# Optimization experiments

Hardware: AMD Instinct MI355X
Metric: run time of the kernel (lower is better)

## Reference

```python
import jax, jax.numpy as jnp
import numpy as np

B, T, D_IN = 512, 128, 256
H1, H2 = 1024, 1024
LABEL_DIM = 3


def _lstm_layer(x, W, U, b):
    """Run one keras-LSTMCell layer over x: [T, B, D_in] -> [T, B, H].

    Keras gate order is (i, f, g, o); c' = f*c + i*tanh(g); h = o*tanh(c').
    """
    H = U.shape[0]
    batch = x.shape[1]

    def step(carry, xt):
        h, c = carry
        z = xt @ W + h @ U + b  # [B, 4H]
        i, f, g, o = jnp.split(z, 4, axis=-1)
        i = jax.nn.sigmoid(i)
        f = jax.nn.sigmoid(f)
        g = jnp.tanh(g)
        o = jax.nn.sigmoid(o)
        c_new = f * c + i * g
        h_new = o * jnp.tanh(c_new)
        return (h_new, c_new), h_new

    init = (jnp.zeros((batch, H), x.dtype), jnp.zeros((batch, H), x.dtype))
    _, hs = jax.lax.scan(step, init, x)
    return hs  # [T, B, H]


def setup_inputs() -> dict:
    key = jax.random.key(0)
    ks = jax.random.split(key, 10)
    chars = jax.random.normal(ks[0], (B, T, D_IN), dtype=jnp.float32)
    # sequence lengths in [1, T] so sequence_length - 1 is a valid index
    sequence_length = jax.random.randint(ks[1], (B,), 1, T + 1)
    s = 0.05
    W1 = jax.random.normal(ks[2], (D_IN, 4 * H1), dtype=jnp.float32) * s
    U1 = jax.random.normal(ks[3], (H1, 4 * H1), dtype=jnp.float32) * s
    b1 = jnp.zeros((4 * H1,), dtype=jnp.float32)
    W2 = jax.random.normal(ks[4], (H1, 4 * H2), dtype=jnp.float32) * s
    U2 = jax.random.normal(ks[5], (H2, 4 * H2), dtype=jnp.float32) * s
    b2 = jnp.zeros((4 * H2,), dtype=jnp.float32)
    Wd = jax.random.normal(ks[6], (H2, LABEL_DIM), dtype=jnp.float32) * s
    bd = jnp.zeros((LABEL_DIM,), dtype=jnp.float32)
    return {"chars": chars, "sequence_length": sequence_length,
            "W1": W1, "U1": U1, "b1": b1,
            "W2": W2, "U2": U2, "b2": b2,
            "Wd": Wd, "bd": bd}


def reference(chars, sequence_length, W1, U1, b1, W2, U2, b2, Wd, bd):
    # chars: [B, T, 256] -> time-major [T, B, 256]
    x = jnp.transpose(chars, (1, 0, 2))
    x = _lstm_layer(x, W1, U1, b1)          # [T, B, H1]
    x = _lstm_layer(x, W2, U2, b2)          # [T, B, H2]
    # gather the hidden state at the last valid timestep of each sequence
    batch = chars.shape[0]
    hidden = x[sequence_length - 1, jnp.arange(batch)]  # [B, H2]
    return jax.nn.relu(hidden @ Wd + bd)    # [B, label_dim]
```

## Files before the change

### kernel.cpp

```cpp
#include <hip/hip_runtime.h>
#include <hip/hip_bf16.h>


typedef __hip_bfloat16 bf16;
typedef __attribute__((ext_vector_type(8))) short bfrag8;
typedef __attribute__((ext_vector_type(4))) float accf4;

#define BATCH 512
#define TSTEPS 128
#define DIN 256
#define H 1024
#define NG 4096

__device__ __forceinline__ float sigm(float x) { return 1.0f / (1.0f + __expf(-x)); }
__device__ __forceinline__ float tanh_f(float x) {
    float a = fabsf(x);
    float e = __expf(-2.0f * a);
    float t = (1.0f - e) / (1.0f + e);
    return x < 0.0f ? -t : t;
}
__device__ __forceinline__ unsigned short bfr16(float x) {
    bf16 h = __float2bfloat16(x);
    return *(unsigned short*)&h;
}
__device__ __forceinline__ void gll16(const void* g, void* l) {
    __builtin_amdgcn_global_load_lds(
        (const __attribute__((address_space(1))) unsigned int*)g,
        (__attribute__((address_space(3))) unsigned int*)l, 16, 0, 0);
}

__global__ void k_repack(const float* __restrict__ W, const float* __restrict__ U,
                         bf16* __restrict__ Bp, int KIN)
{
    __shared__ float tile[128][65];
    int kt = blockIdx.x, nt = blockIdx.y;
    int lane = threadIdx.x;
    int n = nt * 64 + lane;
    int orig = ((n >> 4) & 3) * 1024 + (n >> 7) * 32 + ((n >> 6) & 1) * 16 + (n & 15);
    for (int j = 0; j < 128; ++j) {
        int k = kt * 128 + j;
        tile[j][lane] = (k < KIN) ? W[(size_t)k * NG + orig]
                                  : U[(size_t)(k - KIN) * NG + orig];
    }
    __syncthreads();
    for (int u = 0; u < 16; ++u) {
        int cid = u * 64 + lane;
        int nloc = cid >> 4;
        int pos = cid & 15;
        int nn = nt * 64 + nloc;
        int kc = pos ^ (nn & 7);
        alignas(16) unsigned short pk[8];
        #pragma unroll
        for (int jj = 0; jj < 8; ++jj) pk[jj] = bfr16(tile[kc * 8 + jj][nloc]);
        *(int4*)(Bp + ((size_t)kt * NG + nn) * 128 + pos * 8) = *(int4*)pk;
    }
}

struct StepJob {
    const float* Xf;
    const bf16* A0;
    const bf16* A1;
    const bf16* Bp;
    const float* bias;
    float* C;
    bf16* Hout;
    float* hidden;
    const int* seqlen;
    int xstride;
    int ksplit;
    int KT;
    int t;
};

__global__ __launch_bounds__(256, 2) void k_step(StepJob j0, StepJob j1)
{
    __shared__ __align__(16) bf16 Alds[64 * 128];
    __shared__ __align__(16) bf16 Blds[128 * 128];

    const StepJob jb = (blockIdx.x >> 8) ? j1 : j0;
    int bi = blockIdx.x & 255;
    int tid = threadIdx.x;
    int wv = tid >> 6, lane = tid & 63;
    int ntile = bi & 31;
    int b0 = (bi >> 5) * 64;
    int n0 = ntile * 128;
    int mw = (wv & 1) * 32;
    int nw = (wv >> 1) * 64;
    int c = lane & 15, q = lane >> 4;

    const accf4 zero4 = {0.f, 0.f, 0.f, 0.f};
    accf4 acc[2][4];
    #pragma unroll
    for (int i = 0; i < 2; ++i)
        #pragma unroll
        for (int j = 0; j < 4; ++j) acc[i][j] = zero4;

    for (int kt = 0; kt < jb.KT; ++kt) {
        int k0 = kt << 7;
        if (jb.Xf && k0 < jb.ksplit) {
            #pragma unroll
            for (int uu = 0; uu < 4; ++uu) {
                int u = uu * 256 + tid;
                int r = u >> 4;
                int pos = u & 15;
                int kc = pos ^ (r & 7);
                const float* src = jb.Xf + (size_t)(b0 + r) * jb.xstride + k0 + kc * 8;
                float4 va = *(const float4*)src;
                float4 vb = *(const float4*)(src + 4);
                alignas(16) unsigned short pk[8];
                pk[0] = bfr16(va.x); pk[1] = bfr16(va.y);
                pk[2] = bfr16(va.z); pk[3] = bfr16(va.w);
                pk[4] = bfr16(vb.x); pk[5] = bfr16(vb.y);
                pk[6] = bfr16(vb.z); pk[7] = bfr16(vb.w);
                *(int4*)((char*)Alds + u * 16) = *(int4*)pk;
            }
        } else {
            const bf16* Asrc; int kk0;
            if (k0 < jb.ksplit) { Asrc = jb.A0; kk0 = k0; }
            else                { Asrc = jb.A1; kk0 = k0 - jb.ksplit; }
            #pragma unroll
            for (int cc = 0; cc < 4; ++cc) {
                int ob = wv * 4096 + cc * 1024;
                int o = ob + lane * 16;
                int r = o >> 8;
                const char* g = (const char*)Asrc + (size_t)(b0 + r) * (H * 2) + kk0 * 2 + (o & 255);
                gll16(g, (char*)Alds + ob);
            }
        }
        const char* Bg = (const char*)jb.Bp + ((size_t)kt * NG + n0) * 256;
        #pragma unroll
        for (int cc = 0; cc < 8; ++cc) {
            int ob = wv * 8192 + cc * 1024;
            gll16(Bg + ob + lane * 16, (char*)Blds + ob);
        }
        __syncthreads();
        #pragma unroll
        for (int kk = 0; kk < 128; kk += 32) {
            int kc = (kk >> 3) + q;
            int ra = mw + c;
            int pa = (kc ^ (ra & 7)) << 3;
            bfrag8 af0 = *(const bfrag8*)(Alds + ra * 128 + pa);
            bfrag8 af1 = *(const bfrag8*)(Alds + (ra + 16) * 128 + pa);
            #pragma unroll
            for (int nt = 0; nt < 4; ++nt) {
                int nn = nw + nt * 16 + c;
                bfrag8 bfv = *(const bfrag8*)(Blds + nn * 128 + ((kc ^ (nn & 7)) << 3));
                acc[0][nt] = __builtin_amdgcn_mfma_f32_16x16x32_bf16(af0, bfv, acc[0][nt], 0, 0, 0);
                acc[1][nt] = __builtin_amdgcn_mfma_f32_16x16x32_bf16(af1, bfv, acc[1][nt], 0, 0, 0);
            }
        }
        __syncthreads();
    }

    int hcol = ntile * 32 + (wv >> 1) * 16 + c;
    float bi_ = jb.bias[hcol],         bf_ = jb.bias[H + hcol];
    float bg_ = jb.bias[2 * H + hcol], bo_ = jb.bias[3 * H + hcol];
    int seg = hcol & ~127;
    int kc_ = (hcol & 127) >> 3;
    int jl = hcol & 7;
    #pragma unroll
    for (int mt = 0; mt < 2; ++mt) {
        #pragma unroll
        for (int reg = 0; reg < 4; ++reg) {
            int b = b0 + mw + mt * 16 + q * 4 + reg;
            float ig = sigm(acc[mt][0][reg] + bi_);
            float fg = sigm(acc[mt][1][reg] + bf_);
            float gv = tanh_f(acc[mt][2][reg] + bg_);
            float og = sigm(acc[mt][3][reg] + bo_);
            size_t ci = (size_t)b * H + hcol;
            float cv = fg * jb.C[ci] + ig * gv;
            jb.C[ci] = cv;
            float h = og * tanh_f(cv);
            jb.Hout[(size_t)b * H + seg + ((kc_ ^ (b & 7)) << 3) + jl] = __float2bfloat16(h);
            if (jb.hidden) {
                if (jb.seqlen[b] - 1 == jb.t) jb.hidden[ci] = h;
            }
        }
    }
}

__global__ void k_final(const float* __restrict__ hidden, const float* __restrict__ Wd,
                        const float* __restrict__ bd, float* __restrict__ out)
{
    int b = blockIdx.x;
    int l = threadIdx.x;
    float p0 = 0.f, p1 = 0.f, p2 = 0.f;
    for (int jj = l; jj < H; jj += 64) {
        float hv = hidden[(size_t)b * H + jj];
        p0 += hv * Wd[jj * 3 + 0];
        p1 += hv * Wd[jj * 3 + 1];
        p2 += hv * Wd[jj * 3 + 2];
    }
    #pragma unroll
    for (int off = 32; off > 0; off >>= 1) {
        p0 += __shfl_down(p0, off);
        p1 += __shfl_down(p1, off);
        p2 += __shfl_down(p2, off);
    }
    if (l == 0) {
        out[b * 3 + 0] = fmaxf(p0 + bd[0], 0.f);
        out[b * 3 + 1] = fmaxf(p1 + bd[1], 0.f);
        out[b * 3 + 2] = fmaxf(p2 + bd[2], 0.f);
    }
}

extern "C" void kernel_launch(void* const* d_in, const int* in_sizes, int n_in,
                              void* d_out, int out_size, void* d_ws, size_t ws_size,
                              hipStream_t stream)
{
    const float* chars = (const float*)d_in[0];
    const int* seqlen  = (const int*)d_in[1];
    const float* W1 = (const float*)d_in[2];
    const float* U1 = (const float*)d_in[3];
    const float* b1 = (const float*)d_in[4];
    const float* W2 = (const float*)d_in[5];
    const float* U2 = (const float*)d_in[6];
    const float* b2 = (const float*)d_in[7];
    const float* Wd = (const float*)d_in[8];
    const float* bd = (const float*)d_in[9];
    float* out = (float*)d_out;

    char* ws = (char*)d_ws;
    size_t off = 0;
    bf16* Bp1 = (bf16*)(ws + off); off += (size_t)10 * NG * 128 * 2;
    bf16* Bp2 = (bf16*)(ws + off); off += (size_t)16 * NG * 128 * 2;
    bf16* h1  = (bf16*)(ws + off); off += (size_t)2 * BATCH * H * 2;
    bf16* h2  = (bf16*)(ws + off); off += (size_t)2 * BATCH * H * 2;
    float* c1 = (float*)(ws + off); off += (size_t)BATCH * H * 4;
    float* c2 = (float*)(ws + off); off += (size_t)BATCH * H * 4;
    float* hidden = (float*)(ws + off); off += (size_t)BATCH * H * 4;
    if (ws_size < off) return;

    hipMemsetAsync(h1, 0, (size_t)2 * BATCH * H * 2, stream);
    hipMemsetAsync(h2, 0, (size_t)2 * BATCH * H * 2, stream);
    hipMemsetAsync(c1, 0, (size_t)BATCH * H * 4, stream);
    hipMemsetAsync(c2, 0, (size_t)BATCH * H * 4, stream);

    k_repack<<<dim3(10, 64), 64, 0, stream>>>(W1, U1, Bp1, 256);
    k_repack<<<dim3(16, 64), 64, 0, stream>>>(W2, U2, Bp2, 1024);

    const size_t HS = (size_t)BATCH * H;

    auto mkL1 = [&](int s) {
        StepJob J;
        J.Xf = chars + (size_t)s * DIN;  J.xstride = TSTEPS * DIN;
        J.A0 = nullptr;
        J.A1 = h1 + (size_t)((s + 1) & 1) * HS;
        J.Bp = Bp1; J.bias = b1; J.C = c1;
        J.Hout = h1 + (size_t)(s & 1) * HS;
        J.hidden = nullptr; J.seqlen = nullptr;
        J.ksplit = 256; J.KT = 10; J.t = s;
        return J;
    };
    auto mkL2 = [&](int s) {
        StepJob J;
        J.Xf = nullptr; J.xstride = 0;
        J.A0 = h1 + (size_t)(s & 1) * HS;
        J.A1 = h2 + (size_t)((s + 1) & 1) * HS;
        J.Bp = Bp2; J.bias = b2; J.C = c2;
        J.Hout = h2 + (size_t)(s & 1) * HS;
        J.hidden = hidden; J.seqlen = seqlen;
        J.ksplit = 1024; J.KT = 16; J.t = s;
        return J;
    };

    StepJob first = mkL1(0);
    k_step<<<256, 256, 0, stream>>>(first, first);
    for (int t = 0; t < TSTEPS - 1; ++t) {
        k_step<<<512, 256, 0, stream>>>(mkL2(t), mkL1(t + 1));
    }
    StepJob last = mkL2(TSTEPS - 1);
    k_step<<<256, 256, 0, stream>>>(last, last);
    k_final<<<512, 64, 0, stream>>>(hidden, Wd, bd, out);
}
```

Baseline: 3.660 ms.

## Sort sequences by length and skip batch tiles of finished sequences

A new single-block kernel sorts batch indices by sequence length, longest first, and records for each timestep how many sequences are still active. Each step kernel gathers its input rows through this permutation and returns early for 64-row batch tiles whose sequences have all ended. The last-valid hidden state is written back to its original batch index. This avoids LSTM matmul work on timesteps past each sequence's end, at the cost of one indirect row load and a small sort launch; partially active tiles still do full work.

After: 3.810 ms. +4.1%, slower.

```diff
diff --git a/kernel.cpp b/kernel.cpp
--- a/kernel.cpp
+++ b/kernel.cpp
@@ -54,6 +54,29 @@
         for (int jj = 0; jj < 8; ++jj) pk[jj] = bfr16(tile[kc * 8 + jj][nloc]);
         *(int4*)(Bp + ((size_t)kt * NG + nn) * 128 + pos * 8) = *(int4*)pk;
     }
+}
+
+__global__ void k_sort(const int* __restrict__ seqlen, int* __restrict__ perm,
+                       int* __restrict__ cnt)
+{
+    __shared__ int hist[129];
+    __shared__ int base[129];
+    __shared__ int cur[129];
+    int tid = threadIdx.x;
+    if (tid < 129) { hist[tid] = 0; cur[tid] = 0; }
+    __syncthreads();
+    int len = seqlen[tid];
+    atomicAdd(&hist[len], 1);
+    __syncthreads();
+    if (tid == 0) {
+        int acc = 0;
+        for (int l = 128; l >= 1; --l) { base[l] = acc; acc += hist[l]; }
+        base[0] = acc;
+    }
+    __syncthreads();
+    int pos = base[len] + atomicAdd(&cur[len], 1);
+    perm[pos] = tid;
+    if (tid < 128) cnt[tid] = base[tid];
 }
 
 struct StepJob {
@@ -66,6 +89,8 @@
     bf16* Hout;
     float* hidden;
     const int* seqlen;
+    const int* perm;
+    const int* cnt;
     int xstride;
     int ksplit;
     int KT;
@@ -79,10 +104,12 @@
 
     const StepJob jb = (blockIdx.x >> 8) ? j1 : j0;
     int bi = blockIdx.x & 255;
+    int b0 = (bi >> 5) * 64;
+    if (b0 >= jb.cnt[jb.t]) return;
+
     int tid = threadIdx.x;
     int wv = tid >> 6, lane = tid & 63;
     int ntile = bi & 31;
-    int b0 = (bi >> 5) * 64;
     int n0 = ntile * 128;
     int mw = (wv & 1) * 32;
     int nw = (wv >> 1) * 64;
@@ -104,7 +131,7 @@
                 int r = u >> 4;
                 int pos = u & 15;
                 int kc = pos ^ (r & 7);
-                const float* src = jb.Xf + (size_t)(b0 + r) * jb.xstride + k0 + kc * 8;
+                const float* src = jb.Xf + (size_t)jb.perm[b0 + r] * jb.xstride + k0 + kc * 8;
                 float4 va = *(const float4*)src;
                 float4 vb = *(const float4*)(src + 4);
                 alignas(16) unsigned short pk[8];
@@ -173,7 +200,9 @@
             float h = og * tanh_f(cv);
             jb.Hout[(size_t)b * H + seg + ((kc_ ^ (b & 7)) << 3) + jl] = __float2bfloat16(h);
             if (jb.hidden) {
-                if (jb.seqlen[b] - 1 == jb.t) jb.hidden[ci] = h;
+                int pb = jb.perm[b];
+                if (jb.seqlen[pb] - 1 == jb.t)
+                    jb.hidden[(size_t)pb * H + hcol] = h;
             }
         }
     }
@@ -229,6 +258,8 @@
     float* c1 = (float*)(ws + off); off += (size_t)BATCH * H * 4;
     float* c2 = (float*)(ws + off); off += (size_t)BATCH * H * 4;
     float* hidden = (float*)(ws + off); off += (size_t)BATCH * H * 4;
+    int* perm = (int*)(ws + off); off += BATCH * 4;
+    int* cntA = (int*)(ws + off); off += TSTEPS * 4;
     if (ws_size < off) return;
 
     hipMemsetAsync(h1, 0, (size_t)2 * BATCH * H * 2, stream);
@@ -238,6 +269,7 @@
 
     k_repack<<<dim3(10, 64), 64, 0, stream>>>(W1, U1, Bp1, 256);
     k_repack<<<dim3(16, 64), 64, 0, stream>>>(W2, U2, Bp2, 1024);
+    k_sort<<<1, 512, 0, stream>>>(seqlen, perm, cntA);
 
     const size_t HS = (size_t)BATCH * H;
 
@@ -249,6 +281,7 @@
         J.Bp = Bp1; J.bias = b1; J.C = c1;
         J.Hout = h1 + (size_t)(s & 1) * HS;
         J.hidden = nullptr; J.seqlen = nullptr;
+        J.perm = perm; J.cnt = cntA;
         J.ksplit = 256; J.KT = 10; J.t = s;
         return J;
     };
@@ -260,6 +293,7 @@
         J.Bp = Bp2; J.bias = b2; J.C = c2;
         J.Hout = h2 + (size_t)(s & 1) * HS;
         J.hidden = hidden; J.seqlen = seqlen;
+        J.perm = perm; J.cnt = cntA;
         J.ksplit = 1024; J.KT = 16; J.t = s;
         return J;
     };
```
